# Kernel optimization log

Measured on AMD Instinct MI355X. Metric: run time of the kernel, lower is better.

Reference implementation:

```python
import jax, jax.numpy as jnp
import numpy as np
from jax.ops import segment_sum

N_NODES = 200_000
N_EDGES = 6_400_000


def gcn_conv(x, W, b, src, dst, num_nodes):
    """PyG GCNConv (default): h = x @ W; add self-loops; symmetric norm; scatter-add; + bias."""
    h = x @ W  # [N, F_out]
    loop = jnp.arange(num_nodes, dtype=src.dtype)
    s = jnp.concatenate([src, loop])  # source (message sender)
    d = jnp.concatenate([dst, loop])  # target (aggregation index)
    ones = jnp.ones(s.shape[0], dtype=h.dtype)
    deg = segment_sum(ones, d, num_segments=num_nodes)  # in-degree incl. self-loop
    dinv = jnp.where(deg > 0, jax.lax.rsqrt(deg), 0.0)
    norm = dinv[s] * dinv[d]  # [E+N]
    msg = h[s] * norm[:, None]  # [E+N, F_out]
    out = segment_sum(msg, d, num_segments=num_nodes)
    return out + b


def setup_inputs() -> dict:
    key = jax.random.key(0)
    ks = jax.random.split(key, 6)
    x = jax.random.normal(ks[0], (N_NODES, 6), dtype=jnp.float32)
    edge_index = jax.random.randint(ks[1], (2, N_EDGES), 0, N_NODES, dtype=jnp.int32)
    W1 = jax.random.normal(ks[2], (6, 16), dtype=jnp.float32) * (1.0 / np.sqrt(6))
    b1 = jnp.zeros((16,), dtype=jnp.float32)
    W2 = jax.random.normal(ks[3], (16, 8), dtype=jnp.float32) * (1.0 / np.sqrt(16))
    b2 = jnp.zeros((8,), dtype=jnp.float32)
    Wfc = jax.random.normal(ks[4], (8, 1), dtype=jnp.float32) * (1.0 / np.sqrt(8))
    bfc = jnp.zeros((1,), dtype=jnp.float32)
    return {"x": x, "edge_index": edge_index, "W1": W1, "b1": b1,
            "W2": W2, "b2": b2, "Wfc": Wfc, "bfc": bfc}


def reference(x, edge_index, W1, b1, W2, b2, Wfc, bfc):
    src, dst = edge_index[0], edge_index[1]
    h = gcn_conv(x, W1, b1, src, dst, N_NODES)
    h = jax.nn.relu(h)
    h = gcn_conv(h, W2, b2, src, dst, N_NODES)
    h = jax.nn.relu(h)
    out = h @ Wfc + bfc
    return jax.nn.sigmoid(out)
```

## Files before the change

kernel.cpp:

```cpp
#include <hip/hip_runtime.h>
#include <math.h>


#define TPB 256
#define NBS 8
#define NBKT 256
#define MAXB 1024
#define BPT (MAXB / TPB)
#define CHUNK 4096
#define EPT (CHUNK / TPB)
#define CAP 9216
#define RPT (CAP / TPB)

__device__ __forceinline__ unsigned short f2bf(float f) {
    unsigned u = __float_as_uint(f);
    unsigned r = (u + 0x7FFFu + ((u >> 16) & 1u)) >> 16;
    return (unsigned short)r;
}
__device__ __forceinline__ unsigned pk2(float a, float b) {
    return (unsigned)f2bf(a) | ((unsigned)f2bf(b) << 16);
}
#define BFLO(u) __uint_as_float((u) << 16)
#define BFHI(u) __uint_as_float((u) & 0xFFFF0000u)

__global__ void __launch_bounds__(TPB) k_fb1(
        const int* __restrict__ dst, int* __restrict__ C, int e, int nb) {
    __shared__ int h[MAXB];
    int t = threadIdx.x;
    int c0 = blockIdx.x * CHUNK;
    int csize = min(e - c0, CHUNK);
#pragma unroll
    for (int k = 0; k < BPT; k++) h[t * BPT + k] = 0;
    __syncthreads();
    for (int i = c0 + t; i < c0 + csize; i += TPB)
        atomicAdd(&h[dst[i] >> NBS], 1);
    __syncthreads();
    int* row = C + (size_t)blockIdx.x * nb;
    for (int b = t; b < nb; b += TPB) row[b] = h[b];
}

__global__ void __launch_bounds__(TPB) k_scanC(
        const int* __restrict__ C, int* __restrict__ O, int* __restrict__ btot,
        int nchunk, int nb) {
    __shared__ int sm[TPB];
    int b = blockIdx.x, t = threadIdx.x;
    int run = b * CAP;
    for (int c0 = 0; c0 < nchunk; c0 += TPB) {
        int c = c0 + t;
        int v = (c < nchunk) ? C[(size_t)c * nb + b] : 0;
        sm[t] = v;
        __syncthreads();
        for (int off = 1; off < TPB; off <<= 1) {
            int a = (t >= off) ? sm[t - off] : 0;
            __syncthreads();
            sm[t] += a;
            __syncthreads();
        }
        if (c < nchunk) O[(size_t)c * nb + b] = run + sm[t] - v;
        int tile = sm[TPB - 1];
        __syncthreads();
        run += tile;
    }
    if (t == 0) btot[b] = run - b * CAP;
}

__global__ void __launch_bounds__(TPB) k_fillbin(
        const int* __restrict__ src, const int* __restrict__ dst,
        const int* __restrict__ O, int* __restrict__ binned, int e, int nb) {
    __shared__ int stage[CHUNK];
    __shared__ unsigned short bs[CHUNK];
    __shared__ int h[MAXB];
    __shared__ int excl[MAXB];
    __shared__ int delta[MAXB];
    __shared__ int tmp[TPB];
    int t = threadIdx.x;
    int c0 = blockIdx.x * CHUNK;
    int csize = min(e - c0, CHUNK);
#pragma unroll
    for (int k = 0; k < BPT; k++) h[t * BPT + k] = 0;
    __syncthreads();
    int dreg[EPT];
#pragma unroll
    for (int k = 0; k < EPT; k++) {
        int idx = t + k * TPB;
        int d = (idx < csize) ? dst[c0 + idx] : -1;
        dreg[k] = d;
        if (d >= 0) atomicAdd(&h[d >> NBS], 1);
    }
    __syncthreads();
    int loc[BPT];
    int ts = 0;
#pragma unroll
    for (int k = 0; k < BPT; k++) { loc[k] = ts; ts += h[t * BPT + k]; }
    tmp[t] = ts;
    __syncthreads();
    for (int off = 1; off < TPB; off <<= 1) {
        int a = (t >= off) ? tmp[t - off] : 0;
        __syncthreads();
        tmp[t] += a;
        __syncthreads();
    }
    int tbase = tmp[t] - ts;
#pragma unroll
    for (int k = 0; k < BPT; k++) excl[t * BPT + k] = tbase + loc[k];
    __syncthreads();
    const int* Orow = O + (size_t)blockIdx.x * nb;
#pragma unroll
    for (int k = 0; k < BPT; k++) {
        int b = t * BPT + k;
        delta[b] = ((b < nb) ? Orow[b] : 0) - excl[b];
    }
#pragma unroll
    for (int k = 0; k < BPT; k++) { int b = t * BPT + k; h[b] = excl[b]; }
    __syncthreads();
#pragma unroll
    for (int k = 0; k < EPT; k++) {
        int idx = t + k * TPB;
        if (idx < csize) {
            int d = dreg[k];
            int s = src[c0 + idx];
            int b = d >> NBS;
            int r = atomicAdd(&h[b], 1);
            stage[r] = ((d & (NBKT - 1)) << 18) | s;
            bs[r] = (unsigned short)b;
        }
    }
    __syncthreads();
    for (int k = t; k < csize; k += TPB)
        binned[delta[bs[k]] + k] = stage[k];
}

__global__ void __launch_bounds__(TPB) k_sort(
        const int* __restrict__ binned, const int* __restrict__ btot,
        const float* __restrict__ x, int* __restrict__ csr,
        int* __restrict__ rowptr, int* __restrict__ rowend,
        float* __restrict__ dinv, uint4* __restrict__ xdq, int n) {
    __shared__ int stage[CAP];
    __shared__ int cnt[NBKT];
    __shared__ int excl[NBKT];
    __shared__ int curs[NBKT];
    int b = blockIdx.x, t = threadIdx.x;
    int base = b * CAP;
    int c = btot[b];
    cnt[t] = 0;
    __syncthreads();
    int w[RPT];
#pragma unroll
    for (int k = 0; k < RPT; k++) {
        int idx = t + k * TPB;
        w[k] = (idx < c) ? binned[base + idx] : -1;
        if (w[k] >= 0) atomicAdd(&cnt[w[k] >> 18], 1);
    }
    __syncthreads();
    int v = cnt[t];
    excl[t] = v;
    __syncthreads();
    for (int off = 1; off < NBKT; off <<= 1) {
        int a = (t >= off) ? excl[t - off] : 0;
        __syncthreads();
        excl[t] += a;
        __syncthreads();
    }
    int ex = excl[t] - v;
    curs[t] = ex;
    int i = (b << NBS) + t;
    rowptr[i] = base + ex;
    rowend[i] = base + ex + v;
    if (i < n) {
        float di = rsqrtf((float)(v + 1));
        dinv[i] = di;
        uint4 q;
        q.x = pk2(x[i * 6 + 0] * di, x[i * 6 + 1] * di);
        q.y = pk2(x[i * 6 + 2] * di, x[i * 6 + 3] * di);
        q.z = pk2(x[i * 6 + 4] * di, x[i * 6 + 5] * di);
        q.w = 0;
        xdq[i] = q;
    }
    __syncthreads();
#pragma unroll
    for (int k = 0; k < RPT; k++) {
        if (w[k] >= 0) {
            int r = atomicAdd(&curs[w[k] >> 18], 1);
            stage[r] = w[k] & 0x3FFFF;
        }
    }
    __syncthreads();
    for (int k = t; k < c; k += TPB)
        csr[base + k] = stage[k];
}

__global__ void __launch_bounds__(TPB) k_gat1(
        const uint4* __restrict__ xdq, const int* __restrict__ csr,
        const int* __restrict__ rowptr, const int* __restrict__ rowend,
        const float* __restrict__ dinv,
        const float* __restrict__ b1, const float* __restrict__ W1,
        const float* __restrict__ W2, uint2* __restrict__ g2q, int n) {
    __shared__ float w1[96];
    __shared__ float w2[128];
    __shared__ float bb[16];
    if (threadIdx.x < 96) w1[threadIdx.x] = W1[threadIdx.x];
    if (threadIdx.x < 128) w2[threadIdx.x] = W2[threadIdx.x];
    if (threadIdx.x < 16) bb[threadIdx.x] = b1[threadIdx.x];
    __syncthreads();
    int sub = threadIdx.x & 15;
    int i = blockIdx.x * 16 + (threadIdx.x >> 4);
    bool valid = (i < n);
    int r0 = rowptr[i], r1 = rowend[i];
    float a0 = 0.f, a1 = 0.f, a2 = 0.f, a3 = 0.f, a4 = 0.f, a5 = 0.f;
    float c0 = 0.f, c1 = 0.f, c2 = 0.f, c3 = 0.f, c4 = 0.f, c5 = 0.f;
    if (valid && sub == 0) {
        uint4 q = xdq[i];
        a0 += BFLO(q.x); a1 += BFHI(q.x);
        a2 += BFLO(q.y); a3 += BFHI(q.y);
        a4 += BFLO(q.z); a5 += BFHI(q.z);
    }
    int j = r0 + sub;
    while (j + 16 < r1) {
        uint4 q = xdq[csr[j]];
        uint4 p = xdq[csr[j + 16]];
        a0 += BFLO(q.x); a1 += BFHI(q.x);
        a2 += BFLO(q.y); a3 += BFHI(q.y);
        a4 += BFLO(q.z); a5 += BFHI(q.z);
        c0 += BFLO(p.x); c1 += BFHI(p.x);
        c2 += BFLO(p.y); c3 += BFHI(p.y);
        c4 += BFLO(p.z); c5 += BFHI(p.z);
        j += 32;
    }
    if (j < r1) {
        uint4 q = xdq[csr[j]];
        a0 += BFLO(q.x); a1 += BFHI(q.x);
        a2 += BFLO(q.y); a3 += BFHI(q.y);
        a4 += BFLO(q.z); a5 += BFHI(q.z);
    }
    a0 += c0; a1 += c1; a2 += c2; a3 += c3; a4 += c4; a5 += c5;
#pragma unroll
    for (int m = 1; m <= 8; m <<= 1) {
        a0 += __shfl_xor(a0, m); a1 += __shfl_xor(a1, m);
        a2 += __shfl_xor(a2, m); a3 += __shfl_xor(a3, m);
        a4 += __shfl_xor(a4, m); a5 += __shfl_xor(a5, m);
    }
    float di = valid ? dinv[i] : 0.f;
    int f = sub;
    float hf = a0 * w1[f] + a1 * w1[16 + f] + a2 * w1[32 + f]
             + a3 * w1[48 + f] + a4 * w1[64 + f] + a5 * w1[80 + f];
    float tf = fmaxf(di * hf + bb[f], 0.0f);
    float p0 = tf * w2[f * 8 + 0], p1 = tf * w2[f * 8 + 1];
    float p2 = tf * w2[f * 8 + 2], p3 = tf * w2[f * 8 + 3];
    float p4 = tf * w2[f * 8 + 4], p5 = tf * w2[f * 8 + 5];
    float p6 = tf * w2[f * 8 + 6], p7 = tf * w2[f * 8 + 7];
#pragma unroll
    for (int m = 1; m <= 8; m <<= 1) {
        p0 += __shfl_xor(p0, m); p1 += __shfl_xor(p1, m);
        p2 += __shfl_xor(p2, m); p3 += __shfl_xor(p3, m);
        p4 += __shfl_xor(p4, m); p5 += __shfl_xor(p5, m);
        p6 += __shfl_xor(p6, m); p7 += __shfl_xor(p7, m);
    }
    if (valid && sub < 2) {
        float q0 = sub ? p4 : p0, q1 = sub ? p5 : p1;
        float q2 = sub ? p6 : p2, q3 = sub ? p7 : p3;
        uint2 o;
        o.x = pk2(q0 * di, q1 * di);
        o.y = pk2(q2 * di, q3 * di);
        g2q[i * 2 + sub] = o;
    }
}

__global__ void __launch_bounds__(TPB) k_gat2(
        const uint4* __restrict__ g2q, const int* __restrict__ csr,
        const int* __restrict__ rowptr, const int* __restrict__ rowend,
        const float* __restrict__ dinv,
        const float* __restrict__ b2, const float* __restrict__ Wfc,
        const float* __restrict__ bfc, float* __restrict__ out, int n) {
    __shared__ float w[8];
    __shared__ float bb[8];
    __shared__ float bf;
    if (threadIdx.x < 8) { w[threadIdx.x] = Wfc[threadIdx.x]; bb[threadIdx.x] = b2[threadIdx.x]; }
    if (threadIdx.x == 0) bf = bfc[0];
    __syncthreads();
    int sub = threadIdx.x & 15;
    int i = blockIdx.x * 16 + (threadIdx.x >> 4);
    bool valid = (i < n);
    int r0 = rowptr[i], r1 = rowend[i];
    float a0 = 0.f, a1 = 0.f, a2 = 0.f, a3 = 0.f;
    float a4 = 0.f, a5 = 0.f, a6 = 0.f, a7 = 0.f;
    if (valid && sub == 0) {
        uint4 q = g2q[i];
        a0 += BFLO(q.x); a1 += BFHI(q.x); a2 += BFLO(q.y); a3 += BFHI(q.y);
        a4 += BFLO(q.z); a5 += BFHI(q.z); a6 += BFLO(q.w); a7 += BFHI(q.w);
    }
    float c0 = 0.f, c1 = 0.f, c2 = 0.f, c3 = 0.f;
    float c4 = 0.f, c5 = 0.f, c6 = 0.f, c7 = 0.f;
    int j = r0 + sub;
    while (j + 16 < r1) {
        uint4 q = g2q[csr[j]];
        uint4 p = g2q[csr[j + 16]];
        a0 += BFLO(q.x); a1 += BFHI(q.x); a2 += BFLO(q.y); a3 += BFHI(q.y);
        a4 += BFLO(q.z); a5 += BFHI(q.z); a6 += BFLO(q.w); a7 += BFHI(q.w);
        c0 += BFLO(p.x); c1 += BFHI(p.x); c2 += BFLO(p.y); c3 += BFHI(p.y);
        c4 += BFLO(p.z); c5 += BFHI(p.z); c6 += BFLO(p.w); c7 += BFHI(p.w);
        j += 32;
    }
    if (j < r1) {
        uint4 q = g2q[csr[j]];
        a0 += BFLO(q.x); a1 += BFHI(q.x); a2 += BFLO(q.y); a3 += BFHI(q.y);
        a4 += BFLO(q.z); a5 += BFHI(q.z); a6 += BFLO(q.w); a7 += BFHI(q.w);
    }
    a0 += c0; a1 += c1; a2 += c2; a3 += c3;
    a4 += c4; a5 += c5; a6 += c6; a7 += c7;
#pragma unroll
    for (int m = 1; m <= 8; m <<= 1) {
        a0 += __shfl_xor(a0, m); a1 += __shfl_xor(a1, m);
        a2 += __shfl_xor(a2, m); a3 += __shfl_xor(a3, m);
        a4 += __shfl_xor(a4, m); a5 += __shfl_xor(a5, m);
        a6 += __shfl_xor(a6, m); a7 += __shfl_xor(a7, m);
    }
    if (valid && sub == 0) {
        float di = dinv[i];
        float o = bf;
        o += fmaxf(di * a0 + bb[0], 0.0f) * w[0];
        o += fmaxf(di * a1 + bb[1], 0.0f) * w[1];
        o += fmaxf(di * a2 + bb[2], 0.0f) * w[2];
        o += fmaxf(di * a3 + bb[3], 0.0f) * w[3];
        o += fmaxf(di * a4 + bb[4], 0.0f) * w[4];
        o += fmaxf(di * a5 + bb[5], 0.0f) * w[5];
        o += fmaxf(di * a6 + bb[6], 0.0f) * w[6];
        o += fmaxf(di * a7 + bb[7], 0.0f) * w[7];
        out[i] = 1.0f / (1.0f + expf(-o));
    }
}

extern "C" void kernel_launch(void* const* d_in, const int* in_sizes, int n_in,
                              void* d_out, int out_size, void* d_ws, size_t ws_size,
                              hipStream_t stream) {
    const float* x   = (const float*)d_in[0];
    const int*   ei  = (const int*)d_in[1];
    const float* W1  = (const float*)d_in[2];
    const float* b1  = (const float*)d_in[3];
    const float* W2  = (const float*)d_in[4];
    const float* b2  = (const float*)d_in[5];
    const float* Wfc = (const float*)d_in[6];
    const float* bfc = (const float*)d_in[7];
    float* out = (float*)d_out;

    const int n = in_sizes[0] / 6;
    const int e = in_sizes[1] / 2;
    const int* src = ei;
    const int* dst = ei + e;
    const int nb = (n + NBKT - 1) >> NBS;
    const size_t np = (size_t)nb << NBS;
    const int nblk = (e + CHUNK - 1) / CHUNK;
    const size_t reg = (size_t)nb * CAP;

    int* C      = (int*)d_ws;
    int* O      = C + (size_t)nblk * nb;
    int* btot   = O + (size_t)nblk * nb;
    int* binned = btot + MAXB;
    int* csr    = binned + reg;
    int* rowptr = csr + reg;
    int* rowend = rowptr + np;
    float* dinv = (float*)(rowend + np);
    uint4* xdq  = (uint4*)(dinv + np);
    uint2* g2q  = (uint2*)(xdq + np);

    int gw = (n + 15) / 16;

    k_fb1<<<nblk, TPB, 0, stream>>>(dst, C, e, nb);
    k_scanC<<<nb, TPB, 0, stream>>>(C, O, btot, nblk, nb);
    k_fillbin<<<nblk, TPB, 0, stream>>>(src, dst, O, binned, e, nb);
    k_sort<<<nb, TPB, 0, stream>>>(binned, btot, x, csr, rowptr, rowend, dinv, xdq, n);
    k_gat1<<<gw, TPB, 0, stream>>>(xdq, csr, rowptr, rowend, dinv, b1, W1, W2, g2q, n);
    k_gat2<<<gw, TPB, 0, stream>>>((const uint4*)g2q, csr, rowptr, rowend, dinv, b2, Wfc, bfc, out, n);
}
```

Baseline: 277.1 us.

## Replace count-scan binning passes with global atomic bucket cursors and wave scans

```diff
diff --git a/kernel.cpp b/kernel.cpp
--- a/kernel.cpp
+++ b/kernel.cpp
@@ -11,6 +11,7 @@
 #define EPT (CHUNK / TPB)
 #define CAP 9216
 #define RPT (CAP / TPB)
+#define NWAVE (TPB / 64)
 
 __device__ __forceinline__ unsigned short f2bf(float f) {
     unsigned u = __float_as_uint(f);
@@ -23,56 +24,14 @@
 #define BFLO(u) __uint_as_float((u) << 16)
 #define BFHI(u) __uint_as_float((u) & 0xFFFF0000u)
 
-__global__ void __launch_bounds__(TPB) k_fb1(
-        const int* __restrict__ dst, int* __restrict__ C, int e, int nb) {
-    __shared__ int h[MAXB];
-    int t = threadIdx.x;
-    int c0 = blockIdx.x * CHUNK;
-    int csize = min(e - c0, CHUNK);
-#pragma unroll
-    for (int k = 0; k < BPT; k++) h[t * BPT + k] = 0;
-    __syncthreads();
-    for (int i = c0 + t; i < c0 + csize; i += TPB)
-        atomicAdd(&h[dst[i] >> NBS], 1);
-    __syncthreads();
-    int* row = C + (size_t)blockIdx.x * nb;
-    for (int b = t; b < nb; b += TPB) row[b] = h[b];
-}
-
-__global__ void __launch_bounds__(TPB) k_scanC(
-        const int* __restrict__ C, int* __restrict__ O, int* __restrict__ btot,
-        int nchunk, int nb) {
-    __shared__ int sm[TPB];
-    int b = blockIdx.x, t = threadIdx.x;
-    int run = b * CAP;
-    for (int c0 = 0; c0 < nchunk; c0 += TPB) {
-        int c = c0 + t;
-        int v = (c < nchunk) ? C[(size_t)c * nb + b] : 0;
-        sm[t] = v;
-        __syncthreads();
-        for (int off = 1; off < TPB; off <<= 1) {
-            int a = (t >= off) ? sm[t - off] : 0;
-            __syncthreads();
-            sm[t] += a;
-            __syncthreads();
-        }
-        if (c < nchunk) O[(size_t)c * nb + b] = run + sm[t] - v;
-        int tile = sm[TPB - 1];
-        __syncthreads();
-        run += tile;
-    }
-    if (t == 0) btot[b] = run - b * CAP;
-}
-
 __global__ void __launch_bounds__(TPB) k_fillbin(
         const int* __restrict__ src, const int* __restrict__ dst,
-        const int* __restrict__ O, int* __restrict__ binned, int e, int nb) {
+        int* __restrict__ cur, int* __restrict__ binned, int e, int nb) {
     __shared__ int stage[CHUNK];
     __shared__ unsigned short bs[CHUNK];
     __shared__ int h[MAXB];
-    __shared__ int excl[MAXB];
     __shared__ int delta[MAXB];
-    __shared__ int tmp[TPB];
+    __shared__ int wsum[NWAVE];
     int t = threadIdx.x;
     int c0 = blockIdx.x * CHUNK;
     int csize = min(e - c0, CHUNK);
@@ -88,30 +47,38 @@
         if (d >= 0) atomicAdd(&h[d >> NBS], 1);
     }
     __syncthreads();
-    int loc[BPT];
+    int loc[BPT], hreg[BPT];
     int ts = 0;
 #pragma unroll
-    for (int k = 0; k < BPT; k++) { loc[k] = ts; ts += h[t * BPT + k]; }
-    tmp[t] = ts;
-    __syncthreads();
-    for (int off = 1; off < TPB; off <<= 1) {
-        int a = (t >= off) ? tmp[t - off] : 0;
-        __syncthreads();
-        tmp[t] += a;
-        __syncthreads();
-    }
-    int tbase = tmp[t] - ts;
-#pragma unroll
-    for (int k = 0; k < BPT; k++) excl[t * BPT + k] = tbase + loc[k];
-    __syncthreads();
-    const int* Orow = O + (size_t)blockIdx.x * nb;
+    for (int k = 0; k < BPT; k++) {
+        hreg[k] = h[t * BPT + k];
+        loc[k] = ts;
+        ts += hreg[k];
+    }
+    int lane = t & 63, wid = t >> 6;
+    int v = ts;
+#pragma unroll
+    for (int off = 1; off < 64; off <<= 1) {
+        int u = __shfl_up(v, off);
+        if (lane >= off) v += u;
+    }
+    if (lane == 63) wsum[wid] = v;
+    __syncthreads();
+    int pre = 0;
+#pragma unroll
+    for (int wq = 0; wq < NWAVE - 1; wq++)
+        if (wid > wq) pre += wsum[wq];
+    int tbase = pre + v - ts;
 #pragma unroll
     for (int k = 0; k < BPT; k++) {
         int b = t * BPT + k;
-        delta[b] = ((b < nb) ? Orow[b] : 0) - excl[b];
-    }
-#pragma unroll
-    for (int k = 0; k < BPT; k++) { int b = t * BPT + k; h[b] = excl[b]; }
+        int ex = tbase + loc[k];
+        int d_ = 0;
+        if (hreg[k] > 0)
+            d_ = b * CAP + atomicAdd(&cur[b], hreg[k]) - ex;
+        delta[b] = d_;
+        h[b] = ex;
+    }
     __syncthreads();
 #pragma unroll
     for (int k = 0; k < EPT; k++) {
@@ -137,8 +104,8 @@
         float* __restrict__ dinv, uint4* __restrict__ xdq, int n) {
     __shared__ int stage[CAP];
     __shared__ int cnt[NBKT];
-    __shared__ int excl[NBKT];
     __shared__ int curs[NBKT];
+    __shared__ int wsum[NWAVE];
     int b = blockIdx.x, t = threadIdx.x;
     int base = b * CAP;
     int c = btot[b];
@@ -153,15 +120,20 @@
     }
     __syncthreads();
     int v = cnt[t];
-    excl[t] = v;
-    __syncthreads();
-    for (int off = 1; off < NBKT; off <<= 1) {
-        int a = (t >= off) ? excl[t - off] : 0;
-        __syncthreads();
-        excl[t] += a;
-        __syncthreads();
-    }
-    int ex = excl[t] - v;
+    int lane = t & 63, wid = t >> 6;
+    int iv = v;
+#pragma unroll
+    for (int off = 1; off < 64; off <<= 1) {
+        int u = __shfl_up(iv, off);
+        if (lane >= off) iv += u;
+    }
+    if (lane == 63) wsum[wid] = iv;
+    __syncthreads();
+    int pre = 0;
+#pragma unroll
+    for (int wq = 0; wq < NWAVE - 1; wq++)
+        if (wid > wq) pre += wsum[wq];
+    int ex = pre + iv - v;
     curs[t] = ex;
     int i = (b << NBS) + t;
     rowptr[i] = base + ex;
@@ -351,10 +323,8 @@
     const int nblk = (e + CHUNK - 1) / CHUNK;
     const size_t reg = (size_t)nb * CAP;
 
-    int* C      = (int*)d_ws;
-    int* O      = C + (size_t)nblk * nb;
-    int* btot   = O + (size_t)nblk * nb;
-    int* binned = btot + MAXB;
+    int* cur    = (int*)d_ws;
+    int* binned = cur + MAXB;
     int* csr    = binned + reg;
     int* rowptr = csr + reg;
     int* rowend = rowptr + np;
@@ -364,10 +334,9 @@
 
     int gw = (n + 15) / 16;
 
-    k_fb1<<<nblk, TPB, 0, stream>>>(dst, C, e, nb);
-    k_scanC<<<nb, TPB, 0, stream>>>(C, O, btot, nblk, nb);
-    k_fillbin<<<nblk, TPB, 0, stream>>>(src, dst, O, binned, e, nb);
-    k_sort<<<nb, TPB, 0, stream>>>(binned, btot, x, csr, rowptr, rowend, dinv, xdq, n);
+    hipMemsetAsync(cur, 0, MAXB * sizeof(int), stream);
+    k_fillbin<<<nblk, TPB, 0, stream>>>(src, dst, cur, binned, e, nb);
+    k_sort<<<nb, TPB, 0, stream>>>(binned, cur, x, csr, rowptr, rowend, dinv, xdq, n);
     k_gat1<<<gw, TPB, 0, stream>>>(xdq, csr, rowptr, rowend, dinv, b1, W1, W2, g2q, n);
     k_gat2<<<gw, TPB, 0, stream>>>((const uint4*)g2q, csr, rowptr, rowend, dinv, b2, Wfc, bfc, out, n);
 }
```

After: 331.9 us. 19.8% more time.
